# Kernel optimization log

Hardware: AMD Instinct MI355X
Metric: run time of the kernel (lower is better)

The kernel has to match this reference:

```python
import jax, jax.numpy as jnp
import numpy as np

N = 50000   # nodes
E = 800000  # edges (avg degree 16)
D = 64      # feature dim (input_dim == hidden_dim == output_dim for num_layer=2)
BN_EPS = 1e-5


def setup_inputs() -> dict:
    key = jax.random.key(0)
    ks = jax.random.split(key, 8)
    def lin_w(k, fan_in, fan_out):
        return jax.random.normal(k, (fan_in, fan_out), jnp.float32) / np.sqrt(fan_in).astype(np.float32)
    inp = {
        "x": jax.random.normal(ks[0], (N, D), jnp.float32),
        "edge_index": jax.random.randint(ks[1], (2, E), 0, N),
    }
    ki = 2
    for l in range(2):
        for s in ("a", "b"):
            inp[f"w{l}{s}"] = lin_w(ks[ki], D, D)
            inp[f"b{l}{s}"] = jnp.zeros((D,), jnp.float32)
            inp[f"g{l}{s}"] = jnp.ones((D,), jnp.float32)   # BN gamma
            inp[f"be{l}{s}"] = jnp.zeros((D,), jnp.float32)  # BN beta
            ki += 1
    inp["lin_w"] = lin_w(ks[6], 2 * D, D)  # JK cat of 2 layers -> 2D, final lin -> D
    inp["lin_b"] = jnp.zeros((D,), jnp.float32)
    return inp


def _bn(h, g, b):
    # BatchNorm1d in training mode: batch statistics over the node axis
    m = h.mean(axis=0)
    v = h.var(axis=0)
    return (h - m) * jax.lax.rsqrt(v + BN_EPS) * g + b


def _gin(h, src, dst, w1, b1, g1, be1, w2, b2, g2, be2):
    # GINConv with eps=0: (1+eps)*x_i + sum_{j->i} x_j, then MLP(Lin-BN-ReLU-Lin-BN-ReLU)
    agg = jax.ops.segment_sum(h[src], dst, num_segments=N) + h
    h = jax.nn.relu(_bn(agg @ w1 + b1, g1, be1))
    return jax.nn.relu(_bn(h @ w2 + b2, g2, be2))


def reference(x, edge_index, w0a, b0a, g0a, be0a, w0b, b0b, g0b, be0b,
              w1a, b1a, g1a, be1a, w1b, b1b, g1b, be1b, lin_w, lin_b):
    src, dst = edge_index[0], edge_index[1]
    h1 = _gin(x, src, dst, w0a, b0a, g0a, be0a, w0b, b0b, g0b, be0b)
    h2 = _gin(h1, src, dst, w1a, b1a, g1a, be1a, w1b, b1b, g1b, be1b)
    # JumpingKnowledge 'cat' over the conv outputs (res[1:]), then final linear
    return jnp.concatenate([h1, h2], axis=1) @ lin_w + lin_b
```

## Files before the change

kernel.cpp:

```cpp
#include <hip/hip_runtime.h>
#include <hip/hip_bf16.h>

#define NN 50000
#define NE 800000
#define BN_EPS 1e-5f
#define CHUNK 8192
#define NCH 98
#define NBK 196

typedef __attribute__((ext_vector_type(4))) float f32x4;

__global__ void zero_k(int* __restrict__ p, int n) {
    int i = blockIdx.x * 256 + threadIdx.x;
    if (i < n) p[i] = 0;
}

__global__ void bhist_k(const int* __restrict__ dst, int* __restrict__ bcnt) {
    __shared__ int c[256];
    int t = threadIdx.x;
    c[t] = 0;
    __syncthreads();
    int base = blockIdx.x * CHUNK;
    int n = NE - base; if (n > CHUNK) n = CHUNK;
    for (int i = t; i < n; i += 256) atomicAdd(&c[dst[base + i] >> 8], 1);
    __syncthreads();
    if (c[t]) atomicAdd(&bcnt[t], c[t]);
}

__global__ void bscan_k(const int* __restrict__ bcnt, int* __restrict__ bbase,
                        int* __restrict__ bres, int* __restrict__ off) {
    __shared__ int s[256];
    int t = threadIdx.x;
    int v = bcnt[t];
    s[t] = v;
    __syncthreads();
    for (int d = 1; d < 256; d <<= 1) {
        int u = (t >= d) ? s[t - d] : 0;
        __syncthreads();
        s[t] += u;
        __syncthreads();
    }
    int ex = s[t] - v;
    bbase[t] = ex;
    bres[t] = ex;
    if (t == 0) { bbase[256] = NE; off[NN] = NE; }
}

__global__ void bscatter_k(const int* __restrict__ src, const int* __restrict__ dst,
                           int* __restrict__ bres, int* __restrict__ ebuf) {
    __shared__ int cnt[256], loff[256], lcur[256], gst[256], sc[256];
    __shared__ int packed[CHUNK];
    int t = threadIdx.x;
    cnt[t] = 0;
    __syncthreads();
    int base = blockIdx.x * CHUNK;
    int n = NE - base; if (n > CHUNK) n = CHUNK;
    for (int i = t; i < n; i += 256) atomicAdd(&cnt[dst[base + i] >> 8], 1);
    __syncthreads();
    sc[t] = cnt[t];
    __syncthreads();
    for (int d = 1; d < 256; d <<= 1) {
        int u = (t >= d) ? sc[t - d] : 0;
        __syncthreads();
        sc[t] += u;
        __syncthreads();
    }
    loff[t] = sc[t] - cnt[t];
    lcur[t] = loff[t];
    __syncthreads();
    for (int i = t; i < n; i += 256) {
        int d = dst[base + i];
        int b = d >> 8;
        int p = atomicAdd(&lcur[b], 1);
        packed[p] = src[base + i] | ((d & 255) << 16) | (b << 24);
    }
    __syncthreads();
    if (cnt[t]) gst[t] = atomicAdd(&bres[t], cnt[t]);
    __syncthreads();
    for (int i = t; i < n; i += 256) {
        int v = packed[i];
        int b = (v >> 24) & 255;
        ebuf[gst[b] + i - loff[b]] = v & 0xFFFFFF;
    }
}

__global__ void csr_k(const int* __restrict__ bbase, const int* __restrict__ ebuf,
                      int* __restrict__ off, int* __restrict__ adj) {
    __shared__ int cnt[256], loff[256], lcur[256], sc[256];
    int b = blockIdx.x, t = threadIdx.x;
    int s0 = bbase[b], s1 = bbase[b + 1];
    int n = s1 - s0;
    cnt[t] = 0;
    __syncthreads();
    for (int i = t; i < n; i += 256) atomicAdd(&cnt[(ebuf[s0 + i] >> 16) & 255], 1);
    __syncthreads();
    sc[t] = cnt[t];
    __syncthreads();
    for (int d = 1; d < 256; d <<= 1) {
        int u = (t >= d) ? sc[t - d] : 0;
        __syncthreads();
        sc[t] += u;
        __syncthreads();
    }
    loff[t] = sc[t] - cnt[t];
    lcur[t] = loff[t];
    int node = b * 256 + t;
    if (node < NN) off[node] = s0 + loff[t];
    __syncthreads();
    for (int i = t; i < n; i += 256) {
        int v = ebuf[s0 + i];
        int p = atomicAdd(&lcur[(v >> 16) & 255], 1);
        adj[s0 + p] = v & 0xFFFF;
    }
}

__global__ void gather_k(const float* __restrict__ X, int ldx,
                         const int* __restrict__ off, const int* __restrict__ adj,
                         float* __restrict__ AGG) {
    int node = blockIdx.x * 4 + (threadIdx.x >> 6);
    int lane = threadIdx.x & 63;
    if (node >= NN) return;
    float acc = X[(size_t)node * ldx + lane];
    int s = off[node], e = off[node + 1];
    int p = s;
    for (; p + 8 <= e; p += 8) {
        int j0 = adj[p + 0], j1 = adj[p + 1], j2 = adj[p + 2], j3 = adj[p + 3];
        int j4 = adj[p + 4], j5 = adj[p + 5], j6 = adj[p + 6], j7 = adj[p + 7];
        float v0 = X[(size_t)j0 * ldx + lane];
        float v1 = X[(size_t)j1 * ldx + lane];
        float v2 = X[(size_t)j2 * ldx + lane];
        float v3 = X[(size_t)j3 * ldx + lane];
        float v4 = X[(size_t)j4 * ldx + lane];
        float v5 = X[(size_t)j5 * ldx + lane];
        float v6 = X[(size_t)j6 * ldx + lane];
        float v7 = X[(size_t)j7 * ldx + lane];
        acc += ((v0 + v1) + (v2 + v3)) + ((v4 + v5) + (v6 + v7));
    }
    if (p + 4 <= e) {
        int j0 = adj[p + 0], j1 = adj[p + 1], j2 = adj[p + 2], j3 = adj[p + 3];
        float v0 = X[(size_t)j0 * ldx + lane];
        float v1 = X[(size_t)j1 * ldx + lane];
        float v2 = X[(size_t)j2 * ldx + lane];
        float v3 = X[(size_t)j3 * ldx + lane];
        acc += (v0 + v1) + (v2 + v3);
        p += 4;
    }
    for (; p < e; p++) acc += X[(size_t)adj[p] * ldx + lane];
    AGG[(size_t)node * 64 + lane] = acc;
}

__global__ void gemm64_k(const float* __restrict__ A,
                         const float* __restrict__ W,
                         const float* __restrict__ bias,
                         float* __restrict__ T,
                         float* __restrict__ sums) {
    __shared__ float As[64 * 72];
    __shared__ float Ws[64 * 64];
    __shared__ float lsum[64], lssq[64];
    int tid = threadIdx.x;
    int rowbase = blockIdx.x * 64;
    for (int i = tid; i < 64 * 16; i += 256) {
        int r = i >> 4, kq = i & 15;
        int row = rowbase + r;
        if (row >= NN) row = NN - 1;
        f32x4 v = *(const f32x4*)(A + (size_t)row * 64 + kq * 4);
        #pragma unroll
        for (int q = 0; q < 4; q++) As[(kq * 4 + q) * 72 + r] = v[q];
    }
    for (int i = tid; i < 1024; i += 256) {
        *(f32x4*)(Ws + i * 4) = *(const f32x4*)(W + i * 4);
    }
    if (tid < 64) { lsum[tid] = 0.f; lssq[tid] = 0.f; }
    __syncthreads();

    int ty = tid >> 4, tx = tid & 15;
    float acc[4][4] = {};
    for (int k = 0; k < 64; k++) {
        float a[4], wv[4];
        #pragma unroll
        for (int i = 0; i < 4; i++) a[i] = As[k * 72 + ty * 4 + i];
        #pragma unroll
        for (int j = 0; j < 4; j++) wv[j] = Ws[k * 64 + tx * 4 + j];
        #pragma unroll
        for (int i = 0; i < 4; i++)
            #pragma unroll
            for (int j = 0; j < 4; j++) acc[i][j] += a[i] * wv[j];
    }

    f32x4 bv = *(const f32x4*)(bias + tx * 4);
    float ps[4] = {0.f, 0.f, 0.f, 0.f}, pq[4] = {0.f, 0.f, 0.f, 0.f};
    #pragma unroll
    for (int i = 0; i < 4; i++) {
        int row = rowbase + ty * 4 + i;
        if (row < NN) {
            f32x4 v;
            #pragma unroll
            for (int j = 0; j < 4; j++) {
                v[j] = acc[i][j] + bv[j];
                ps[j] += v[j];
                pq[j] += v[j] * v[j];
            }
            *(f32x4*)(T + (size_t)row * 64 + tx * 4) = v;
        }
    }
    #pragma unroll
    for (int j = 0; j < 4; j++) {
        atomicAdd(&lsum[tx * 4 + j], ps[j]);
        atomicAdd(&lssq[tx * 4 + j], pq[j]);
    }
    __syncthreads();
    if (tid < 64) {
        atomicAdd(&sums[tid], lsum[tid]);
        atomicAdd(&sums[64 + tid], lssq[tid]);
    }
}

__global__ void gemm64bn_k(const float* __restrict__ Tin,
                           const float* __restrict__ stats,
                           const float* __restrict__ g,
                           const float* __restrict__ be,
                           const float* __restrict__ W,
                           const float* __restrict__ bias,
                           float* __restrict__ T,
                           float* __restrict__ sums) {
    __shared__ float As[64 * 72];
    __shared__ float Ws[64 * 64];
    __shared__ float sc[64], sh[64];
    __shared__ float lsum[64], lssq[64];
    int tid = threadIdx.x;
    int rowbase = blockIdx.x * 64;
    if (tid < 64) {
        float m = stats[tid] * (1.0f / NN);
        float var = stats[64 + tid] * (1.0f / NN) - m * m;
        if (var < 0.f) var = 0.f;
        float s = g[tid] * rsqrtf(var + BN_EPS);
        sc[tid] = s;
        sh[tid] = be[tid] - m * s;
        lsum[tid] = 0.f;
        lssq[tid] = 0.f;
    }
    __syncthreads();
    for (int i = tid; i < 64 * 16; i += 256) {
        int r = i >> 4, kq = i & 15;
        int row = rowbase + r;
        if (row >= NN) row = NN - 1;
        f32x4 v = *(const f32x4*)(Tin + (size_t)row * 64 + kq * 4);
        #pragma unroll
        for (int q = 0; q < 4; q++) {
            int k = kq * 4 + q;
            float u = v[q] * sc[k] + sh[k];
            As[k * 72 + r] = u > 0.f ? u : 0.f;
        }
    }
    for (int i = tid; i < 1024; i += 256) {
        *(f32x4*)(Ws + i * 4) = *(const f32x4*)(W + i * 4);
    }
    __syncthreads();

    int ty = tid >> 4, tx = tid & 15;
    float acc[4][4] = {};
    for (int k = 0; k < 64; k++) {
        float a[4], wv[4];
        #pragma unroll
        for (int i = 0; i < 4; i++) a[i] = As[k * 72 + ty * 4 + i];
        #pragma unroll
        for (int j = 0; j < 4; j++) wv[j] = Ws[k * 64 + tx * 4 + j];
        #pragma unroll
        for (int i = 0; i < 4; i++)
            #pragma unroll
            for (int j = 0; j < 4; j++) acc[i][j] += a[i] * wv[j];
    }

    f32x4 bv = *(const f32x4*)(bias + tx * 4);
    float ps[4] = {0.f, 0.f, 0.f, 0.f}, pq[4] = {0.f, 0.f, 0.f, 0.f};
    #pragma unroll
    for (int i = 0; i < 4; i++) {
        int row = rowbase + ty * 4 + i;
        if (row < NN) {
            f32x4 v;
            #pragma unroll
            for (int j = 0; j < 4; j++) {
                v[j] = acc[i][j] + bv[j];
                ps[j] += v[j];
                pq[j] += v[j] * v[j];
            }
            *(f32x4*)(T + (size_t)row * 64 + tx * 4) = v;
        }
    }
    #pragma unroll
    for (int j = 0; j < 4; j++) {
        atomicAdd(&lsum[tx * 4 + j], ps[j]);
        atomicAdd(&lssq[tx * 4 + j], pq[j]);
    }
    __syncthreads();
    if (tid < 64) {
        atomicAdd(&sums[tid], lsum[tid]);
        atomicAdd(&sums[64 + tid], lssq[tid]);
    }
}

__global__ void bn_k(const float* __restrict__ T, const float* __restrict__ sums,
                     const float* __restrict__ g,
                     const float* __restrict__ be,
                     float* __restrict__ H, int ldh) {
    __shared__ float sc[64], sh[64];
    int tid = threadIdx.x;
    if (tid < 64) {
        float m = sums[tid] * (1.0f / NN);
        float var = sums[64 + tid] * (1.0f / NN) - m * m;
        if (var < 0.f) var = 0.f;
        float s = g[tid] * rsqrtf(var + BN_EPS);
        sc[tid] = s;
        sh[tid] = be[tid] - m * s;
    }
    __syncthreads();
    int i = blockIdx.x * 256 + tid;
    if (i < NN * 16) {
        int row = i >> 4, f = (i & 15) * 4;
        f32x4 v = *(const f32x4*)(T + (size_t)row * 64 + f);
        f32x4 u;
        #pragma unroll
        for (int j = 0; j < 4; j++) {
            float w = v[j] * sc[f + j] + sh[f + j];
            u[j] = w > 0.f ? w : 0.f;
        }
        *(f32x4*)(H + (size_t)row * ldh + f) = u;
    }
}

__global__ void gemmfin_k(const float* __restrict__ A,
                          const float* __restrict__ W,
                          const float* __restrict__ bias,
                          float* __restrict__ O) {
    __shared__ float As[128 * 72];
    __shared__ float Ws[128 * 64];
    int tid = threadIdx.x;
    int rowbase = blockIdx.x * 64;
    for (int i = tid; i < 64 * 32; i += 256) {
        int r = i >> 5, kq = i & 31;
        int row = rowbase + r;
        if (row >= NN) row = NN - 1;
        f32x4 v = *(const f32x4*)(A + (size_t)row * 128 + kq * 4);
        #pragma unroll
        for (int q = 0; q < 4; q++) As[(kq * 4 + q) * 72 + r] = v[q];
    }
    for (int i = tid; i < 2048; i += 256) {
        *(f32x4*)(Ws + i * 4) = *(const f32x4*)(W + i * 4);
    }
    __syncthreads();

    int ty = tid >> 4, tx = tid & 15;
    float acc[4][4] = {};
    for (int k = 0; k < 128; k++) {
        float a[4], wv[4];
        #pragma unroll
        for (int i = 0; i < 4; i++) a[i] = As[k * 72 + ty * 4 + i];
        #pragma unroll
        for (int j = 0; j < 4; j++) wv[j] = Ws[k * 64 + tx * 4 + j];
        #pragma unroll
        for (int i = 0; i < 4; i++)
            #pragma unroll
            for (int j = 0; j < 4; j++) acc[i][j] += a[i] * wv[j];
    }

    f32x4 bv = *(const f32x4*)(bias + tx * 4);
    #pragma unroll
    for (int i = 0; i < 4; i++) {
        int row = rowbase + ty * 4 + i;
        if (row < NN) {
            f32x4 v;
            #pragma unroll
            for (int j = 0; j < 4; j++) v[j] = acc[i][j] + bv[j];
            *(f32x4*)(O + (size_t)row * 64 + tx * 4) = v;
        }
    }
}

extern "C" void kernel_launch(void* const* d_in, const int* in_sizes, int n_in,
                              void* d_out, int out_size, void* d_ws, size_t ws_size,
                              hipStream_t stream) {
    const float* x   = (const float*)d_in[0];
    const int*   ei  = (const int*)d_in[1];
    const float* w0a = (const float*)d_in[2];
    const float* b0a = (const float*)d_in[3];
    const float* g0a = (const float*)d_in[4];
    const float* be0a= (const float*)d_in[5];
    const float* w0b = (const float*)d_in[6];
    const float* b0b = (const float*)d_in[7];
    const float* g0b = (const float*)d_in[8];
    const float* be0b= (const float*)d_in[9];
    const float* w1a = (const float*)d_in[10];
    const float* b1a = (const float*)d_in[11];
    const float* g1a = (const float*)d_in[12];
    const float* be1a= (const float*)d_in[13];
    const float* w1b = (const float*)d_in[14];
    const float* b1b = (const float*)d_in[15];
    const float* g1b = (const float*)d_in[16];
    const float* be1b= (const float*)d_in[17];
    const float* lw  = (const float*)d_in[18];
    const float* lb  = (const float*)d_in[19];
    float* out = (float*)d_out;
    (void)in_sizes; (void)n_in; (void)out_size; (void)ws_size;

    char* wsb = (char*)d_ws;
    size_t o = 0;
    auto alloc = [&](size_t bytes) -> char* {
        char* p = wsb + o;
        o += (bytes + 255) & ~(size_t)255;
        return p;
    };
    int* bcnt = (int*)alloc(256 * 4);
    float* sums = (float*)alloc(512 * 4);
    int* bbase = (int*)alloc(257 * 4);
    int* bres = (int*)alloc(256 * 4);
    int* off = (int*)alloc((NN + 1) * 4);
    int* adj = (int*)alloc(NE * 4);
    int* ebuf = (int*)alloc(NE * 4);
    float* AGG = (float*)alloc((size_t)NN * 64 * 4);
    float* T   = (float*)alloc((size_t)NN * 64 * 4);
    float* T2  = (float*)alloc((size_t)NN * 64 * 4);
    float* HC  = (float*)alloc((size_t)NN * 128 * 4);

    const int* src = ei;
    const int* dst = ei + NE;

    zero_k<<<3, 256, 0, stream>>>((int*)d_ws, 768);
    bhist_k<<<NCH, 256, 0, stream>>>(dst, bcnt);
    bscan_k<<<1, 256, 0, stream>>>(bcnt, bbase, bres, off);
    bscatter_k<<<NCH, 256, 0, stream>>>(src, dst, bres, ebuf);
    csr_k<<<NBK, 256, 0, stream>>>(bbase, ebuf, off, adj);

    const int ggrid = NN / 4;
    const int mgrid = (NN + 63) / 64;
    const int agrid = (NN * 16 + 255) / 256;

    gather_k<<<ggrid, 256, 0, stream>>>(x, 64, off, adj, AGG);
    gemm64_k<<<mgrid, 256, 0, stream>>>(AGG, w0a, b0a, T, sums + 0);
    gemm64bn_k<<<mgrid, 256, 0, stream>>>(T, sums + 0, g0a, be0a, w0b, b0b, T2, sums + 128);
    bn_k<<<agrid, 256, 0, stream>>>(T2, sums + 128, g0b, be0b, HC, 128);

    gather_k<<<ggrid, 256, 0, stream>>>(HC, 128, off, adj, AGG);
    gemm64_k<<<mgrid, 256, 0, stream>>>(AGG, w1a, b1a, T, sums + 256);
    gemm64bn_k<<<mgrid, 256, 0, stream>>>(T, sums + 256, g1a, be1a, w1b, b1b, T2, sums + 384);
    bn_k<<<agrid, 256, 0, stream>>>(T2, sums + 384, g1b, be1b, HC + 64, 128);

    gemmfin_k<<<mgrid, 256, 0, stream>>>(HC, lw, lb, out);
}
```

Before: 370.3 us.

## Fuse neighbor gather into first GEMM and final BN into output GEMM

The neighbor-sum gather now runs inside the first linear-layer kernel: each of the four wavefronts gathers 16 node rows straight into shared memory, so the AGG round trip through global memory and one launch per layer go away. The last BatchNorm+ReLU is folded into the final JK linear kernel, which reads H1 and the raw T2 and normalizes on load, removing a bn pass and the 128-wide concat buffer. The cost is lower gather parallelism, since 782 blocks each serialize 16 rows per wavefront instead of many small blocks hiding latency, and the larger shared-memory footprint may reduce occupancy.

```diff
diff --git a/kernel.cpp b/kernel.cpp
--- a/kernel.cpp
+++ b/kernel.cpp
@@ -114,12 +114,9 @@
     }
 }
 
-__global__ void gather_k(const float* __restrict__ X, int ldx,
-                         const int* __restrict__ off, const int* __restrict__ adj,
-                         float* __restrict__ AGG) {
-    int node = blockIdx.x * 4 + (threadIdx.x >> 6);
-    int lane = threadIdx.x & 63;
-    if (node >= NN) return;
+__device__ __forceinline__ float gather_row(const float* __restrict__ X, int ldx,
+                                            int lane, const int* __restrict__ off,
+                                            const int* __restrict__ adj, int node) {
     float acc = X[(size_t)node * ldx + lane];
     int s = off[node], e = off[node + 1];
     int p = s;
@@ -146,45 +143,47 @@
         p += 4;
     }
     for (; p < e; p++) acc += X[(size_t)adj[p] * ldx + lane];
-    AGG[(size_t)node * 64 + lane] = acc;
-}
-
-__global__ void gemm64_k(const float* __restrict__ A,
-                         const float* __restrict__ W,
-                         const float* __restrict__ bias,
-                         float* __restrict__ T,
-                         float* __restrict__ sums) {
-    __shared__ float As[64 * 72];
+    return acc;
+}
+
+__global__ void ggemm_k(const float* __restrict__ X, int ldx,
+                        const int* __restrict__ off, const int* __restrict__ adj,
+                        const float* __restrict__ W,
+                        const float* __restrict__ bias,
+                        float* __restrict__ T,
+                        float* __restrict__ sums) {
+    __shared__ float As[64 * 65];
     __shared__ float Ws[64 * 64];
     __shared__ float lsum[64], lssq[64];
     int tid = threadIdx.x;
     int rowbase = blockIdx.x * 64;
-    for (int i = tid; i < 64 * 16; i += 256) {
-        int r = i >> 4, kq = i & 15;
-        int row = rowbase + r;
-        if (row >= NN) row = NN - 1;
-        f32x4 v = *(const f32x4*)(A + (size_t)row * 64 + kq * 4);
-        #pragma unroll
-        for (int q = 0; q < 4; q++) As[(kq * 4 + q) * 72 + r] = v[q];
-    }
+    int wv = tid >> 6, lane = tid & 63;
+
     for (int i = tid; i < 1024; i += 256) {
         *(f32x4*)(Ws + i * 4) = *(const f32x4*)(W + i * 4);
     }
     if (tid < 64) { lsum[tid] = 0.f; lssq[tid] = 0.f; }
+
+    for (int rr = 0; rr < 16; rr++) {
+        int r = wv * 16 + rr;
+        int node = rowbase + r;
+        if (node >= NN) node = NN - 1;
+        As[lane * 65 + r] = gather_row(X, ldx, lane, off, adj, node);
+    }
     __syncthreads();
 
     int ty = tid >> 4, tx = tid & 15;
     float acc[4][4] = {};
     for (int k = 0; k < 64; k++) {
-        float a[4], wv[4];
-        #pragma unroll
-        for (int i = 0; i < 4; i++) a[i] = As[k * 72 + ty * 4 + i];
-        #pragma unroll
-        for (int j = 0; j < 4; j++) wv[j] = Ws[k * 64 + tx * 4 + j];
+        float a[4], wvv[4];
+        #pragma unroll
+        for (int i = 0; i < 4; i++) a[i] = As[k * 65 + ty * 4 + i];
+        #pragma unroll
+        for (int j = 0; j < 4; j++) wvv[j] = Ws[k * 64 + tx * 4 + j];
         #pragma unroll
         for (int i = 0; i < 4; i++)
             #pragma unroll
-            for (int j = 0; j < 4; j++) acc[i][j] += a[i] * wv[j];
+            for (int j = 0; j < 4; j++) acc[i][j] += a[i] * wvv[j];
     }
 
     f32x4 bv = *(const f32x4*)(bias + tx * 4);
@@ -302,7 +301,7 @@
 __global__ void bn_k(const float* __restrict__ T, const float* __restrict__ sums,
                      const float* __restrict__ g,
                      const float* __restrict__ be,
-                     float* __restrict__ H, int ldh) {
+                     float* __restrict__ H) {
     __shared__ float sc[64], sh[64];
     int tid = threadIdx.x;
     if (tid < 64) {
@@ -324,25 +323,45 @@
             float w = v[j] * sc[f + j] + sh[f + j];
             u[j] = w > 0.f ? w : 0.f;
         }
-        *(f32x4*)(H + (size_t)row * ldh + f) = u;
-    }
-}
-
-__global__ void gemmfin_k(const float* __restrict__ A,
-                          const float* __restrict__ W,
-                          const float* __restrict__ bias,
-                          float* __restrict__ O) {
+        *(f32x4*)(H + (size_t)row * 64 + f) = u;
+    }
+}
+
+__global__ void gemmfin2_k(const float* __restrict__ H1,
+                           const float* __restrict__ T2,
+                           const float* __restrict__ stats,
+                           const float* __restrict__ g,
+                           const float* __restrict__ be,
+                           const float* __restrict__ W,
+                           const float* __restrict__ bias,
+                           float* __restrict__ O) {
     __shared__ float As[128 * 72];
     __shared__ float Ws[128 * 64];
+    __shared__ float sc[64], sh[64];
     int tid = threadIdx.x;
     int rowbase = blockIdx.x * 64;
-    for (int i = tid; i < 64 * 32; i += 256) {
-        int r = i >> 5, kq = i & 31;
+    if (tid < 64) {
+        float m = stats[tid] * (1.0f / NN);
+        float var = stats[64 + tid] * (1.0f / NN) - m * m;
+        if (var < 0.f) var = 0.f;
+        float s = g[tid] * rsqrtf(var + BN_EPS);
+        sc[tid] = s;
+        sh[tid] = be[tid] - m * s;
+    }
+    __syncthreads();
+    for (int i = tid; i < 64 * 16; i += 256) {
+        int r = i >> 4, kq = i & 15;
         int row = rowbase + r;
         if (row >= NN) row = NN - 1;
-        f32x4 v = *(const f32x4*)(A + (size_t)row * 128 + kq * 4);
-        #pragma unroll
-        for (int q = 0; q < 4; q++) As[(kq * 4 + q) * 72 + r] = v[q];
+        f32x4 v1 = *(const f32x4*)(H1 + (size_t)row * 64 + kq * 4);
+        f32x4 v2 = *(const f32x4*)(T2 + (size_t)row * 64 + kq * 4);
+        #pragma unroll
+        for (int q = 0; q < 4; q++) {
+            int k = kq * 4 + q;
+            As[k * 72 + r] = v1[q];
+            float u = v2[q] * sc[k] + sh[k];
+            As[(64 + k) * 72 + r] = u > 0.f ? u : 0.f;
+        }
     }
     for (int i = tid; i < 2048; i += 256) {
         *(f32x4*)(Ws + i * 4) = *(const f32x4*)(W + i * 4);
@@ -416,10 +435,9 @@
     int* off = (int*)alloc((NN + 1) * 4);
     int* adj = (int*)alloc(NE * 4);
     int* ebuf = (int*)alloc(NE * 4);
-    float* AGG = (float*)alloc((size_t)NN * 64 * 4);
     float* T   = (float*)alloc((size_t)NN * 64 * 4);
     float* T2  = (float*)alloc((size_t)NN * 64 * 4);
-    float* HC  = (float*)alloc((size_t)NN * 128 * 4);
+    float* HC  = (float*)alloc((size_t)NN * 64 * 4);
 
     const int* src = ei;
     const int* dst = ei + NE;
@@ -430,19 +448,15 @@
     bscatter_k<<<NCH, 256, 0, stream>>>(src, dst, bres, ebuf);
     csr_k<<<NBK, 256, 0, stream>>>(bbase, ebuf, off, adj);
 
-    const int ggrid = NN / 4;
     const int mgrid = (NN + 63) / 64;
     const int agrid = (NN * 16 + 255) / 256;
 
-    gather_k<<<ggrid, 256, 0, stream>>>(x, 64, off, adj, AGG);
-    gemm64_k<<<mgrid, 256, 0, stream>>>(AGG, w0a, b0a, T, sums + 0);
+    ggemm_k<<<mgrid, 256, 0, stream>>>(x, 64, off, adj, w0a, b0a, T, sums + 0);
     gemm64bn_k<<<mgrid, 256, 0, stream>>>(T, sums + 0, g0a, be0a, w0b, b0b, T2, sums + 128);
-    bn_k<<<agrid, 256, 0, stream>>>(T2, sums + 128, g0b, be0b, HC, 128);
-
-    gather_k<<<ggrid, 256, 0, stream>>>(HC, 128, off, adj, AGG);
-    gemm64_k<<<mgrid, 256, 0, stream>>>(AGG, w1a, b1a, T, sums + 256);
+    bn_k<<<agrid, 256, 0, stream>>>(T2, sums + 128, g0b, be0b, HC);
+
+    ggemm_k<<<mgrid, 256, 0, stream>>>(HC, 64, off, adj, w1a, b1a, T, sums + 256);
     gemm64bn_k<<<mgrid, 256, 0, stream>>>(T, sums + 256, g1a, be1a, w1b, b1b, T2, sums + 384);
-    bn_k<<<agrid, 256, 0, stream>>>(T2, sums + 384, g1b, be1b, HC + 64, 128);
-
-    gemmfin_k<<<mgrid, 256, 0, stream>>>(HC, lw, lb, out);
-}
+
+    gemmfin2_k<<<mgrid, 256, 0, stream>>>(HC, T2, sums + 384, g1b, be1b, lw, lb, out);
+}
```

Result: slower. 380.0 us (+2.6%).
